# Performance work log

Measured on AMD Instinct MI355X. Metric: run time of the kernel, lower is better.

## Reference

```python
import jax, jax.numpy as jnp
import numpy as np

N_ENT = 100000
N_USR = 1024
E = 400000
D = 128
H = 4
R = 32


def setup_inputs() -> dict:
    key = jax.random.key(0)
    ks = jax.random.split(key, 9)
    a = float(np.sqrt(6.0 / (D + D)))  # xavier_uniform bound for [D, D]
    return {
        "entity_emb": jax.random.normal(ks[0], (N_ENT, D), dtype=jnp.float32),
        "user_emb": jax.random.normal(ks[1], (N_USR, D), dtype=jnp.float32),
        "interact_mat": jnp.zeros((1,), dtype=jnp.float32),  # unused by forward
        "weight": jax.random.normal(ks[2], (R, D), dtype=jnp.float32) * 0.1,
        "qTrans": jax.random.uniform(ks[3], (D, D), minval=-a, maxval=a, dtype=jnp.float32),
        "kTrans": jax.random.uniform(ks[4], (D, D), minval=-a, maxval=a, dtype=jnp.float32),
        "vTrans": jax.random.uniform(ks[5], (D, D), minval=-a, maxval=a, dtype=jnp.float32),
        "edge_index": jax.random.randint(ks[6], (2, E), 0, N_ENT, dtype=jnp.int64)
            if jax.config.jax_enable_x64 else jax.random.randint(ks[6], (2, E), 0, N_ENT, dtype=jnp.int32),
        "edge_type": jax.random.randint(ks[7], (E,), 1, R + 1, dtype=jnp.int32),  # types in [1, R]
        "layer": 0,
    }


def _kglayer(rows, col_embeds, embeds, n_seg, qT, kT, vT):
    # rows: [E] target-node index, col_embeds: [E, D] edge messages
    dh = D // H
    row_embeds = embeds[rows]                              # gather [E, D]
    q = (row_embeds @ qT).reshape(-1, H, dh)
    k = (col_embeds @ kT).reshape(-1, H, dh)
    v = (col_embeds @ vT).reshape(-1, H, dh)
    att = jnp.clip(jnp.einsum("ehd,ehd->eh", q, k), -10.0, 10.0)
    exp_att = jnp.exp(att)                                 # [E, H]
    att_norm = jax.ops.segment_sum(exp_att, rows, num_segments=n_seg)[rows]
    att = exp_att / (att_norm + 1e-8)
    res = (att[..., None] * v).reshape(-1, D)              # [E, D]
    return jax.ops.segment_sum(res, rows, num_segments=n_seg)


def _sim_hrt(head_emb, tail_emb, rel_emb):
    # per-edge scalar attention logit [E, 1]
    tr = jnp.linalg.norm(tail_emb * rel_emb, axis=1, keepdims=True)
    hr = jnp.linalg.norm(head_emb * rel_emb, axis=1, keepdims=True)
    return (hr * tr) ** 2


def reference(entity_emb, user_emb, interact_mat, weight, qTrans, kTrans, vTrans,
              edge_index, edge_type, layer):
    n_entities = entity_emb.shape[0]
    head, tail = edge_index[0], edge_index[1]
    rel = weight[edge_type - 1]                            # [E, D]
    neigh = entity_emb[tail] * rel                         # [E, D]
    kg_emb = _kglayer(head, neigh, entity_emb, n_entities, qTrans, kTrans, vTrans)
    w = _sim_hrt(kg_emb[head], kg_emb[tail], rel)          # [E, 1]
    w = jnp.broadcast_to(w, neigh.shape)                   # expand to [E, D]
    # scatter_softmax over edges sharing the same head (numerically stable)
    m = jax.ops.segment_max(w, head, num_segments=n_entities)[head]
    e = jnp.exp(w - m)
    s = jax.ops.segment_sum(e, head, num_segments=n_entities)[head]
    soft = e / s
    msg = soft * entity_emb[tail]
    return jax.ops.segment_sum(msg, head, num_segments=n_entities)
```

## Files before the change

kernel.cpp:

```cpp
#include <hip/hip_runtime.h>
#include <cstdint>

#define D 128
#define H 4
#define N_ENT 100000
#define N_EDGE 400000
#define R 32

#define SCAN_NB ((N_ENT + 511) / 512)

__global__ void k_hist(const int* __restrict__ head, int* __restrict__ deg) {
  const int e = blockIdx.x * 256 + threadIdx.x;
  if (e < N_EDGE) atomicAdd(&deg[head[e]], 1);
}

__global__ __launch_bounds__(256) void k_scan1(const int* __restrict__ deg,
                                               int* __restrict__ bsum) {
  const int t = threadIdx.x;
  const int i = blockIdx.x * 512 + t * 2;
  int v0 = (i < N_ENT) ? deg[i] : 0;
  int v1 = (i + 1 < N_ENT) ? deg[i + 1] : 0;
  int s = v0 + v1;
#pragma unroll
  for (int k = 1; k < 64; k <<= 1) s += __shfl_xor(s, k);
  __shared__ int ws[4];
  if ((t & 63) == 0) ws[t >> 6] = s;
  __syncthreads();
  if (t == 0) bsum[blockIdx.x] = ws[0] + ws[1] + ws[2] + ws[3];
}

__global__ __launch_bounds__(256) void k_scan2(const int* __restrict__ bsum,
                                               int* __restrict__ bbase,
                                               int* __restrict__ off) {
  __shared__ int sh[256];
  const int t = threadIdx.x;
  const int v = (t < SCAN_NB) ? bsum[t] : 0;
  sh[t] = v;
  __syncthreads();
  for (int d = 1; d < 256; d <<= 1) {
    const int u = (t >= d) ? sh[t - d] : 0;
    __syncthreads();
    sh[t] += u;
    __syncthreads();
  }
  if (t < SCAN_NB) bbase[t] = sh[t] - v;
  if (t == SCAN_NB - 1) off[N_ENT] = sh[t];
}

__global__ __launch_bounds__(256) void k_scan3(const int* __restrict__ deg,
                                               const int* __restrict__ bbase,
                                               int* __restrict__ off,
                                               int* __restrict__ cur) {
  __shared__ int sh[256];
  const int t = threadIdx.x;
  const int i = blockIdx.x * 512 + t * 2;
  const int v0 = (i < N_ENT) ? deg[i] : 0;
  const int v1 = (i + 1 < N_ENT) ? deg[i + 1] : 0;
  const int s = v0 + v1;
  sh[t] = s;
  __syncthreads();
  for (int d = 1; d < 256; d <<= 1) {
    const int u = (t >= d) ? sh[t - d] : 0;
    __syncthreads();
    sh[t] += u;
    __syncthreads();
  }
  const int ex = sh[t] - s + bbase[blockIdx.x];
  if (i < N_ENT) {
    off[i] = ex;
    cur[i] = ex;
  }
  if (i + 1 < N_ENT) {
    off[i + 1] = ex + v0;
    cur[i + 1] = ex + v0;
  }
}

__global__ void k_scatter(const int* __restrict__ head,
                          const int* __restrict__ tail,
                          const int* __restrict__ etype, int* __restrict__ cur,
                          int2* __restrict__ teP) {
  const int e = blockIdx.x * 256 + threadIdx.x;
  if (e >= N_EDGE) return;
  const int hd = head[e];
  const int pos = atomicAdd(&cur[hd], 1);
  teP[pos] = make_int2(tail[e], etype[e] - 1);
}

__global__ __launch_bounds__(256) void k_tr(const float* __restrict__ in,
                                            float* __restrict__ out) {
  __shared__ float tile[32][33];
  const int bx = blockIdx.x & 3, by = blockIdx.x >> 2;
  const int c = threadIdx.x & 31;
  const int r0 = (threadIdx.x >> 5) * 4;
#pragma unroll
  for (int i = 0; i < 4; ++i)
    tile[r0 + i][c] = in[(by * 32 + r0 + i) * 128 + bx * 32 + c];
  __syncthreads();
#pragma unroll
  for (int i = 0; i < 4; ++i)
    out[(bx * 32 + r0 + i) * 128 + by * 32 + c] = tile[c][r0 + i];
}

__global__ __launch_bounds__(512) void k_qproj(const float* __restrict__ ent,
                                               const float* __restrict__ qT,
                                               float* __restrict__ Q) {
  __shared__ float sT[D * D];
  __shared__ float rows[D * 128];
  const int t = threadIdx.x;
  const int n0 = blockIdx.x * 128;
#pragma unroll
  for (int s = 0; s < 8; ++s) {
    const int idx = (s * 512 + t) * 4;
    *(float4*)&sT[idx] = *(const float4*)&qT[idx];
  }
  {
    const int g = t & 3;
    const int n = t >> 2;
    const int node = n0 + n;
    if (node < N_ENT) {
      const float* src = ent + (size_t)node * D;
#pragma unroll
      for (int s = 0; s < 8; ++s) {
        const int i = s * 16 + g * 4;
        float4 v = *(const float4*)&src[i];
        rows[(i + 0) * 128 + n] = v.x;
        rows[(i + 1) * 128 + n] = v.y;
        rows[(i + 2) * 128 + n] = v.z;
        rows[(i + 3) * 128 + n] = v.w;
      }
    } else {
#pragma unroll
      for (int s = 0; s < 8; ++s) {
        const int i = s * 16 + g * 4;
        rows[(i + 0) * 128 + n] = 0.f;
        rows[(i + 1) * 128 + n] = 0.f;
        rows[(i + 2) * 128 + n] = 0.f;
        rows[(i + 3) * 128 + n] = 0.f;
      }
    }
  }
  __syncthreads();
  const int jj = t & 15;
  const int ee = t >> 4;
  float acc[4][8];
#pragma unroll
  for (int a = 0; a < 4; ++a)
#pragma unroll
    for (int b = 0; b < 8; ++b) acc[a][b] = 0.f;
#pragma unroll 4
  for (int i = 0; i < D; ++i) {
    float4 b0 = *(float4*)&sT[i * D + jj * 8];
    float4 b1 = *(float4*)&sT[i * D + jj * 8 + 4];
    float4 a0 = *(float4*)&rows[i * 128 + ee * 4];
    float bv[8] = {b0.x, b0.y, b0.z, b0.w, b1.x, b1.y, b1.z, b1.w};
    float av[4] = {a0.x, a0.y, a0.z, a0.w};
#pragma unroll
    for (int a = 0; a < 4; ++a)
#pragma unroll
      for (int b = 0; b < 8; ++b) acc[a][b] = fmaf(av[a], bv[b], acc[a][b]);
  }
#pragma unroll
  for (int a = 0; a < 4; ++a) {
    const int node = n0 + ee * 4 + a;
    if (node < N_ENT) {
      float4 o0 = {acc[a][0], acc[a][1], acc[a][2], acc[a][3]};
      float4 o1 = {acc[a][4], acc[a][5], acc[a][6], acc[a][7]};
      *(float4*)&Q[(size_t)node * D + jj * 8] = o0;
      *(float4*)&Q[(size_t)node * D + jj * 8 + 4] = o1;
    }
  }
}

__global__ __launch_bounds__(256, 8) void k_fused(
    const float* __restrict__ ent, const float* __restrict__ wrel,
    const float* __restrict__ kTt, const float* __restrict__ vT, float* qkg,
    const int* __restrict__ off, const int2* __restrict__ teP) {
  __shared__ float sQ[8 * 128];
  __shared__ float sPA[8 * 512];
  const int t = threadIdx.x;
  const int base = blockIdx.x * 8;

  const int wid = t >> 6;
  const int half = (t >> 5) & 1;
  const int l32 = t & 31;
  const int kk = wid * 2 + half;
  const int n = base + kk;

  {
    const int k = t >> 5;
    const int c4 = (t & 31) * 4;
    *(float4*)&sQ[k * 128 + c4] =
        *(const float4*)&qkg[(size_t)(base + k) * D + c4];
  }

  const int eb = off[n];
  const int deg = off[n + 1] - eb;
  float4 xv = {0, 0, 0, 0}, rv = {0, 0, 0, 0};
  if (deg > 0) {
    const int2 pf = teP[eb];
    xv = *(const float4*)&ent[(size_t)pf.x * D + l32 * 4];
    rv = *(const float4*)&wrel[(size_t)pf.y * D + l32 * 4];
  }
  __syncthreads();

  {
    const int i = t & 127;
    const int sub = t >> 7;
    float pp[2][8];
#pragma unroll
    for (int hh = 0; hh < 2; ++hh)
#pragma unroll
      for (int k = 0; k < 8; ++k) pp[hh][k] = 0.f;
#pragma unroll
    for (int hh = 0; hh < 2; ++hh) {
      const int h = sub * 2 + hh;
#pragma unroll 2
      for (int c4 = 0; c4 < 8; ++c4) {
        const float kv0 = kTt[(h * 32 + c4 * 4 + 0) * 128 + i];
        const float kv1 = kTt[(h * 32 + c4 * 4 + 1) * 128 + i];
        const float kv2 = kTt[(h * 32 + c4 * 4 + 2) * 128 + i];
        const float kv3 = kTt[(h * 32 + c4 * 4 + 3) * 128 + i];
#pragma unroll
        for (int k = 0; k < 8; ++k) {
          const float4 q = *(const float4*)&sQ[k * 128 + h * 32 + c4 * 4];
          pp[hh][k] = fmaf(kv0, q.x, pp[hh][k]);
          pp[hh][k] = fmaf(kv1, q.y, pp[hh][k]);
          pp[hh][k] = fmaf(kv2, q.z, pp[hh][k]);
          pp[hh][k] = fmaf(kv3, q.w, pp[hh][k]);
        }
      }
    }
#pragma unroll
    for (int hh = 0; hh < 2; ++hh)
#pragma unroll
      for (int k = 0; k < 8; ++k)
        sPA[k * 512 + (sub * 2 + hh) * 128 + i] = pp[hh][k];
  }
  __syncthreads();

  {
    const int lp = l32 & 3;
    const float4 P0 = *(const float4*)&sPA[kk * 512 + 0 * 128 + l32 * 4];
    const float4 P1 = *(const float4*)&sPA[kk * 512 + 1 * 128 + l32 * 4];
    const float4 P2 = *(const float4*)&sPA[kk * 512 + 2 * 128 + l32 * 4];
    const float4 P3 = *(const float4*)&sPA[kk * 512 + 3 * 128 + l32 * 4];
    float4 b0 = {0, 0, 0, 0}, b1 = {0, 0, 0, 0};
    float4 b2 = {0, 0, 0, 0}, b3 = {0, 0, 0, 0};
    float s0 = 0.f, s1 = 0.f, s2 = 0.f, s3 = 0.f;
    for (int idx = 0; idx < deg; ++idx) {
      const float4 cx = xv, cr = rv;
      if (idx + 1 < deg) {
        const int2 pf = teP[eb + idx + 1];
        xv = *(const float4*)&ent[(size_t)pf.x * D + l32 * 4];
        rv = *(const float4*)&wrel[(size_t)pf.y * D + l32 * 4];
      }
      const float4 nh = {cx.x * cr.x, cx.y * cr.y, cx.z * cr.z, cx.w * cr.w};
      float d0 = nh.x * P0.x + nh.y * P0.y + nh.z * P0.z + nh.w * P0.w;
      float d1 = nh.x * P1.x + nh.y * P1.y + nh.z * P1.z + nh.w * P1.w;
      float d2 = nh.x * P2.x + nh.y * P2.y + nh.z * P2.z + nh.w * P2.w;
      float d3 = nh.x * P3.x + nh.y * P3.y + nh.z * P3.z + nh.w * P3.w;
      float x01 = (l32 & 1) ? d1 : d0;
      float y01 = (l32 & 1) ? d0 : d1;
      x01 += __shfl_xor(y01, 1);
      float x23 = (l32 & 1) ? d3 : d2;
      float y23 = (l32 & 1) ? d2 : d3;
      x23 += __shfl_xor(y23, 1);
      float xa = (l32 & 2) ? x23 : x01;
      float xb = (l32 & 2) ? x01 : x23;
      xa += __shfl_xor(xb, 2);
      xa += __shfl_xor(xa, 4);
      xa += __shfl_xor(xa, 8);
      xa += __shfl_xor(xa, 16);
      const float eL = __expf(fminf(fmaxf(xa, -10.f), 10.f));
      const float e0 = eL;
      const float e1 = __shfl_xor(eL, 1);
      const float e2 = __shfl_xor(eL, 2);
      const float e3 = __shfl_xor(eL, 3);
      b0.x = fmaf(e0, nh.x, b0.x); b0.y = fmaf(e0, nh.y, b0.y);
      b0.z = fmaf(e0, nh.z, b0.z); b0.w = fmaf(e0, nh.w, b0.w);
      b1.x = fmaf(e1, nh.x, b1.x); b1.y = fmaf(e1, nh.y, b1.y);
      b1.z = fmaf(e1, nh.z, b1.z); b1.w = fmaf(e1, nh.w, b1.w);
      b2.x = fmaf(e2, nh.x, b2.x); b2.y = fmaf(e2, nh.y, b2.y);
      b2.z = fmaf(e2, nh.z, b2.z); b2.w = fmaf(e2, nh.w, b2.w);
      b3.x = fmaf(e3, nh.x, b3.x); b3.y = fmaf(e3, nh.y, b3.y);
      b3.z = fmaf(e3, nh.z, b3.z); b3.w = fmaf(e3, nh.w, b3.w);
      s0 += e0; s1 += e1; s2 += e2; s3 += e3;
    }
    const float i0 = 1.f / (s0 + 1e-8f);
    const float i1 = 1.f / (s1 + 1e-8f);
    const float i2 = 1.f / (s2 + 1e-8f);
    const float i3 = 1.f / (s3 + 1e-8f);
    float4 o0 = {b0.x * i0, b0.y * i0, b0.z * i0, b0.w * i0};
    float4 o1 = {b1.x * i1, b1.y * i1, b1.z * i1, b1.w * i1};
    float4 o2 = {b2.x * i2, b2.y * i2, b2.z * i2, b2.w * i2};
    float4 o3 = {b3.x * i3, b3.y * i3, b3.z * i3, b3.w * i3};
    const int sb = kk * 512 + l32 * 4;
    *(float4*)&sPA[sb + ((lp ^ 0) << 7)] = o0;
    *(float4*)&sPA[sb + ((lp ^ 1) << 7)] = o1;
    *(float4*)&sPA[sb + ((lp ^ 2) << 7)] = o2;
    *(float4*)&sPA[sb + ((lp ^ 3) << 7)] = o3;
  }
  __syncthreads();

  {
    const int c = t & 127;
    const int g4 = (t >> 7) * 4;
    const int h = c >> 5;
    float acc0 = 0.f, acc1 = 0.f, acc2 = 0.f, acc3 = 0.f;
    const float* agg0 = &sPA[(g4 + 0) * 512 + h * 128];
    const float* agg1 = &sPA[(g4 + 1) * 512 + h * 128];
    const float* agg2 = &sPA[(g4 + 2) * 512 + h * 128];
    const float* agg3 = &sPA[(g4 + 3) * 512 + h * 128];
#pragma unroll 4
    for (int d4 = 0; d4 < 32; ++d4) {
      const float4 a0 = *(const float4*)&agg0[d4 * 4];
      const float4 a1 = *(const float4*)&agg1[d4 * 4];
      const float4 a2 = *(const float4*)&agg2[d4 * 4];
      const float4 a3 = *(const float4*)&agg3[d4 * 4];
      const float v0 = vT[(d4 * 4 + 0) * 128 + c];
      const float v1 = vT[(d4 * 4 + 1) * 128 + c];
      const float v2 = vT[(d4 * 4 + 2) * 128 + c];
      const float v3 = vT[(d4 * 4 + 3) * 128 + c];
      acc0 = fmaf(a0.x, v0, acc0); acc0 = fmaf(a0.y, v1, acc0);
      acc0 = fmaf(a0.z, v2, acc0); acc0 = fmaf(a0.w, v3, acc0);
      acc1 = fmaf(a1.x, v0, acc1); acc1 = fmaf(a1.y, v1, acc1);
      acc1 = fmaf(a1.z, v2, acc1); acc1 = fmaf(a1.w, v3, acc1);
      acc2 = fmaf(a2.x, v0, acc2); acc2 = fmaf(a2.y, v1, acc2);
      acc2 = fmaf(a2.z, v2, acc2); acc2 = fmaf(a2.w, v3, acc2);
      acc3 = fmaf(a3.x, v0, acc3); acc3 = fmaf(a3.y, v1, acc3);
      acc3 = fmaf(a3.z, v2, acc3); acc3 = fmaf(a3.w, v3, acc3);
    }
    qkg[(size_t)(base + g4 + 0) * D + c] = acc0;
    qkg[(size_t)(base + g4 + 1) * D + c] = acc1;
    qkg[(size_t)(base + g4 + 2) * D + c] = acc2;
    qkg[(size_t)(base + g4 + 3) * D + c] = acc3;
  }
}

__global__ __launch_bounds__(256) void k_S(const float* __restrict__ kg,
                                           const float* __restrict__ wrel,
                                           float* __restrict__ S) {
  __shared__ float sB[D * 32];
  __shared__ float sA[D * 64];
  const int t = threadIdx.x;
  const int n0 = blockIdx.x * 64;
  {
    const int r = t & 31;
    const int qg = t >> 5;
#pragma unroll
    for (int s = 0; s < 4; ++s) {
      const int d = qg * 16 + s * 4;
      float4 b = *(const float4*)&wrel[(size_t)r * D + d];
      sB[(d + 0) * 32 + r] = b.x * b.x;
      sB[(d + 1) * 32 + r] = b.y * b.y;
      sB[(d + 2) * 32 + r] = b.z * b.z;
      sB[(d + 3) * 32 + r] = b.w * b.w;
    }
  }
  {
    const int nn = t & 63;
    const int dg = t >> 6;
    const int node = n0 + nn;
#pragma unroll
    for (int s = 0; s < 8; ++s) {
      const int d = dg * 32 + s * 4;
      float4 a = {0, 0, 0, 0};
      if (node < N_ENT) a = *(const float4*)&kg[(size_t)node * D + d];
      sA[(d + 0) * 64 + nn] = a.x * a.x;
      sA[(d + 1) * 64 + nn] = a.y * a.y;
      sA[(d + 2) * 64 + nn] = a.z * a.z;
      sA[(d + 3) * 64 + nn] = a.w * a.w;
    }
  }
  __syncthreads();
  const int nn2 = t >> 2;
  const int rg = t & 3;
  float acc[8];
#pragma unroll
  for (int c = 0; c < 8; ++c) acc[c] = 0.f;
#pragma unroll 4
  for (int d = 0; d < D; ++d) {
    const float a = sA[d * 64 + nn2];
    float4 b0 = *(float4*)&sB[d * 32 + rg * 8];
    float4 b1 = *(float4*)&sB[d * 32 + rg * 8 + 4];
    acc[0] = fmaf(a, b0.x, acc[0]);
    acc[1] = fmaf(a, b0.y, acc[1]);
    acc[2] = fmaf(a, b0.z, acc[2]);
    acc[3] = fmaf(a, b0.w, acc[3]);
    acc[4] = fmaf(a, b1.x, acc[4]);
    acc[5] = fmaf(a, b1.y, acc[5]);
    acc[6] = fmaf(a, b1.z, acc[6]);
    acc[7] = fmaf(a, b1.w, acc[7]);
  }
  const int node = n0 + nn2;
  if (node < N_ENT) {
    float4 o0 = {acc[0], acc[1], acc[2], acc[3]};
    float4 o1 = {acc[4], acc[5], acc[6], acc[7]};
    *(float4*)&S[(size_t)node * 32 + rg * 8] = o0;
    *(float4*)&S[(size_t)node * 32 + rg * 8 + 4] = o1;
  }
}

__global__ __launch_bounds__(256) void k_out2(
    const float* __restrict__ ent, const float* __restrict__ S,
    const int* __restrict__ off, const int2* __restrict__ teP,
    float* __restrict__ out) {
  const int t = threadIdx.x;
  const int wid = t >> 6;
  const int lane = t & 63;
  const int n = blockIdx.x * 4 + wid;
  if (n >= N_ENT) return;
  const int eb = off[n];
  const int deg = off[n + 1] - eb;
  float accx = 0.f, accy = 0.f;
  float m = 0.f, ssum = 0.f;
  for (int b = 0; b < deg; b += 64) {
    const int idx = b + lane;
    const bool val = idx < deg;
    const int e = eb + (val ? idx : 0);
    const int2 tp = teP[e];
    const int tl = tp.x;
    const int ty = tp.y;
    float w = val ? S[(size_t)n * 32 + ty] * S[(size_t)tl * 32 + ty] : -1.f;
    float cm = w;
#pragma unroll
    for (int k = 1; k < 64; k <<= 1) cm = fmaxf(cm, __shfl_xor(cm, k));
    const float mnew = fmaxf(m, cm);
    const float scale = __expf(m - mnew);
    const float el = val ? __expf(w - mnew) : 0.f;
    float cs = el;
#pragma unroll
    for (int k = 1; k < 64; k <<= 1) cs += __shfl_xor(cs, k);
    ssum = ssum * scale + cs;
    accx *= scale;
    accy *= scale;
    const int cnt = (deg - b < 64) ? deg - b : 64;
    {
      const int tl0 = __shfl(tl, 0);
      float2 xr = *(const float2*)&ent[(size_t)tl0 * D + lane * 2];
      for (int j = 0; j < cnt; ++j) {
        const float sj = __shfl(el, j);
        const float2 cx = xr;
        if (j + 1 < cnt) {
          const int tlj = __shfl(tl, j + 1);
          xr = *(const float2*)&ent[(size_t)tlj * D + lane * 2];
        }
        accx = fmaf(sj, cx.x, accx);
        accy = fmaf(sj, cx.y, accy);
      }
    }
    m = mnew;
  }
  const float inv = (deg > 0) ? 1.f / ssum : 0.f;
  float2 o = {accx * inv, accy * inv};
  *(float2*)&out[(size_t)n * D + lane * 2] = o;
}

extern "C" void kernel_launch(void* const* d_in, const int* in_sizes, int n_in,
                              void* d_out, int out_size, void* d_ws,
                              size_t ws_size, hipStream_t stream) {
  const float* ent = (const float*)d_in[0];
  const float* wrel = (const float*)d_in[3];
  const float* qT = (const float*)d_in[4];
  const float* kT = (const float*)d_in[5];
  const float* vT = (const float*)d_in[6];
  const int* eidx = (const int*)d_in[7];
  const int* etype = (const int*)d_in[8];
  const int* head = eidx;
  const int* tail = eidx + N_EDGE;

  float* S = (float*)d_ws;
  int* off = (int*)(S + (size_t)N_ENT * 32);
  int* cur = off + (N_ENT + 2);
  int* deg = cur + N_ENT;
  int* bsum = deg + N_ENT;
  int* bbase = bsum + SCAN_NB;
  int2* teP = (int2*)(bbase + SCAN_NB);
  float* kTt = (float*)(teP + N_EDGE);
  float* qkg = (float*)d_out;

  hipMemsetAsync(deg, 0, N_ENT * sizeof(int), stream);
  k_hist<<<(N_EDGE + 255) / 256, 256, 0, stream>>>(head, deg);
  k_scan1<<<SCAN_NB, 256, 0, stream>>>(deg, bsum);
  k_scan2<<<1, 256, 0, stream>>>(bsum, bbase, off);
  k_scan3<<<SCAN_NB, 256, 0, stream>>>(deg, bbase, off, cur);
  k_scatter<<<(N_EDGE + 255) / 256, 256, 0, stream>>>(head, tail, etype, cur,
                                                      teP);
  k_tr<<<16, 256, 0, stream>>>(kT, kTt);
  k_qproj<<<(N_ENT + 127) / 128, 512, 0, stream>>>(ent, qT, qkg);
  k_fused<<<N_ENT / 8, 256, 0, stream>>>(ent, wrel, kTt, vT, qkg, off, teP);
  k_S<<<(N_ENT + 63) / 64, 256, 0, stream>>>(qkg, wrel, S);
  k_out2<<<(N_ENT + 3) / 4, 256, 0, stream>>>(ent, S, off, teP, qkg);
}
```

Baseline: 512.1 us.

## Fuse relation-similarity matrix into attention kernel and narrow output gather to half-waves

The per-node S = kg^2 · wrel^2 computation moves into the tail of k_fused, using squared kg values kept in shared memory, so the kg embedding no longer round-trips through global memory for a separate k_S launch. Squared relation weights are precomputed once in a merged prep kernel that reuses the transpose launch. k_out2 now handles 8 nodes per block with 32-lane groups using float4 loads instead of 64-lane float2. The P vectors are also reloaded from LDS each iteration rather than held in registers, which may lower register pressure but adds LDS traffic. The S dot product in k_fused is unblocked (one scalar per thread over 128 values), which costs extra ALU and LDS work in that kernel.

```diff
diff --git a/kernel.cpp b/kernel.cpp
--- a/kernel.cpp
+++ b/kernel.cpp
@@ -87,19 +87,32 @@
   teP[pos] = make_int2(tail[e], etype[e] - 1);
 }
 
-__global__ __launch_bounds__(256) void k_tr(const float* __restrict__ in,
-                                            float* __restrict__ out) {
-  __shared__ float tile[32][33];
-  const int bx = blockIdx.x & 3, by = blockIdx.x >> 2;
-  const int c = threadIdx.x & 31;
-  const int r0 = (threadIdx.x >> 5) * 4;
-#pragma unroll
-  for (int i = 0; i < 4; ++i)
-    tile[r0 + i][c] = in[(by * 32 + r0 + i) * 128 + bx * 32 + c];
-  __syncthreads();
-#pragma unroll
-  for (int i = 0; i < 4; ++i)
-    out[(bx * 32 + r0 + i) * 128 + by * 32 + c] = tile[c][r0 + i];
+__global__ __launch_bounds__(256) void k_prep(const float* __restrict__ kT,
+                                              float* __restrict__ kTt,
+                                              const float* __restrict__ wrel,
+                                              float* __restrict__ wrel2) {
+  if (blockIdx.x < 16) {
+    __shared__ float tile[32][33];
+    const int bx = blockIdx.x & 3, by = blockIdx.x >> 2;
+    const int c = threadIdx.x & 31;
+    const int r0 = (threadIdx.x >> 5) * 4;
+#pragma unroll
+    for (int i = 0; i < 4; ++i)
+      tile[r0 + i][c] = kT[(by * 32 + r0 + i) * 128 + bx * 32 + c];
+    __syncthreads();
+#pragma unroll
+    for (int i = 0; i < 4; ++i)
+      kTt[(bx * 32 + r0 + i) * 128 + by * 32 + c] = tile[c][r0 + i];
+  } else {
+    const int t = threadIdx.x;
+#pragma unroll
+    for (int s = 0; s < 4; ++s) {
+      const int idx = (s * 256 + t) * 4;
+      float4 v = *(const float4*)&wrel[idx];
+      v.x *= v.x; v.y *= v.y; v.z *= v.z; v.w *= v.w;
+      *(float4*)&wrel2[idx] = v;
+    }
+  }
 }
 
 __global__ __launch_bounds__(512) void k_qproj(const float* __restrict__ ent,
@@ -174,13 +187,14 @@
 
 __global__ __launch_bounds__(256, 8) void k_fused(
     const float* __restrict__ ent, const float* __restrict__ wrel,
-    const float* __restrict__ kTt, const float* __restrict__ vT, float* qkg,
-    const int* __restrict__ off, const int2* __restrict__ teP) {
+    const float* __restrict__ kTt, const float* __restrict__ vT,
+    const float* __restrict__ wrel2, const float* __restrict__ qkg,
+    float* __restrict__ S, const int* __restrict__ off,
+    const int2* __restrict__ teP) {
   __shared__ float sQ[8 * 128];
   __shared__ float sPA[8 * 512];
   const int t = threadIdx.x;
   const int base = blockIdx.x * 8;
-
   const int wid = t >> 6;
   const int half = (t >> 5) & 1;
   const int l32 = t & 31;
@@ -241,25 +255,25 @@
 
   {
     const int lp = l32 & 3;
-    const float4 P0 = *(const float4*)&sPA[kk * 512 + 0 * 128 + l32 * 4];
-    const float4 P1 = *(const float4*)&sPA[kk * 512 + 1 * 128 + l32 * 4];
-    const float4 P2 = *(const float4*)&sPA[kk * 512 + 2 * 128 + l32 * 4];
-    const float4 P3 = *(const float4*)&sPA[kk * 512 + 3 * 128 + l32 * 4];
+    const float* Pb = &sPA[kk * 512 + l32 * 4];
     float4 b0 = {0, 0, 0, 0}, b1 = {0, 0, 0, 0};
     float4 b2 = {0, 0, 0, 0}, b3 = {0, 0, 0, 0};
     float s0 = 0.f, s1 = 0.f, s2 = 0.f, s3 = 0.f;
     for (int idx = 0; idx < deg; ++idx) {
-      const float4 cx = xv, cr = rv;
+      const float4 nh = {xv.x * rv.x, xv.y * rv.y, xv.z * rv.z, xv.w * rv.w};
       if (idx + 1 < deg) {
         const int2 pf = teP[eb + idx + 1];
         xv = *(const float4*)&ent[(size_t)pf.x * D + l32 * 4];
         rv = *(const float4*)&wrel[(size_t)pf.y * D + l32 * 4];
       }
-      const float4 nh = {cx.x * cr.x, cx.y * cr.y, cx.z * cr.z, cx.w * cr.w};
-      float d0 = nh.x * P0.x + nh.y * P0.y + nh.z * P0.z + nh.w * P0.w;
-      float d1 = nh.x * P1.x + nh.y * P1.y + nh.z * P1.z + nh.w * P1.w;
-      float d2 = nh.x * P2.x + nh.y * P2.y + nh.z * P2.z + nh.w * P2.w;
-      float d3 = nh.x * P3.x + nh.y * P3.y + nh.z * P3.z + nh.w * P3.w;
+      const float4 p0 = *(const float4*)&Pb[0];
+      const float4 p1 = *(const float4*)&Pb[128];
+      const float4 p2 = *(const float4*)&Pb[256];
+      const float4 p3 = *(const float4*)&Pb[384];
+      float d0 = nh.x * p0.x + nh.y * p0.y + nh.z * p0.z + nh.w * p0.w;
+      float d1 = nh.x * p1.x + nh.y * p1.y + nh.z * p1.z + nh.w * p1.w;
+      float d2 = nh.x * p2.x + nh.y * p2.y + nh.z * p2.z + nh.w * p2.w;
+      float d3 = nh.x * p3.x + nh.y * p3.y + nh.z * p3.z + nh.w * p3.w;
       float x01 = (l32 & 1) ? d1 : d0;
       float y01 = (l32 & 1) ? d0 : d1;
       x01 += __shfl_xor(y01, 1);
@@ -331,74 +345,27 @@
       acc3 = fmaf(a3.x, v0, acc3); acc3 = fmaf(a3.y, v1, acc3);
       acc3 = fmaf(a3.z, v2, acc3); acc3 = fmaf(a3.w, v3, acc3);
     }
-    qkg[(size_t)(base + g4 + 0) * D + c] = acc0;
-    qkg[(size_t)(base + g4 + 1) * D + c] = acc1;
-    qkg[(size_t)(base + g4 + 2) * D + c] = acc2;
-    qkg[(size_t)(base + g4 + 3) * D + c] = acc3;
-  }
-}
-
-__global__ __launch_bounds__(256) void k_S(const float* __restrict__ kg,
-                                           const float* __restrict__ wrel,
-                                           float* __restrict__ S) {
-  __shared__ float sB[D * 32];
-  __shared__ float sA[D * 64];
-  const int t = threadIdx.x;
-  const int n0 = blockIdx.x * 64;
-  {
+    sQ[(g4 + 0) * 128 + c] = acc0 * acc0;
+    sQ[(g4 + 1) * 128 + c] = acc1 * acc1;
+    sQ[(g4 + 2) * 128 + c] = acc2 * acc2;
+    sQ[(g4 + 3) * 128 + c] = acc3 * acc3;
+  }
+  __syncthreads();
+
+  {
+    const int nn = t >> 5;
     const int r = t & 31;
-    const int qg = t >> 5;
-#pragma unroll
-    for (int s = 0; s < 4; ++s) {
-      const int d = qg * 16 + s * 4;
-      float4 b = *(const float4*)&wrel[(size_t)r * D + d];
-      sB[(d + 0) * 32 + r] = b.x * b.x;
-      sB[(d + 1) * 32 + r] = b.y * b.y;
-      sB[(d + 2) * 32 + r] = b.z * b.z;
-      sB[(d + 3) * 32 + r] = b.w * b.w;
-    }
-  }
-  {
-    const int nn = t & 63;
-    const int dg = t >> 6;
-    const int node = n0 + nn;
-#pragma unroll
-    for (int s = 0; s < 8; ++s) {
-      const int d = dg * 32 + s * 4;
-      float4 a = {0, 0, 0, 0};
-      if (node < N_ENT) a = *(const float4*)&kg[(size_t)node * D + d];
-      sA[(d + 0) * 64 + nn] = a.x * a.x;
-      sA[(d + 1) * 64 + nn] = a.y * a.y;
-      sA[(d + 2) * 64 + nn] = a.z * a.z;
-      sA[(d + 3) * 64 + nn] = a.w * a.w;
-    }
-  }
-  __syncthreads();
-  const int nn2 = t >> 2;
-  const int rg = t & 3;
-  float acc[8];
-#pragma unroll
-  for (int c = 0; c < 8; ++c) acc[c] = 0.f;
+    const float* kg2 = &sQ[nn * 128];
+    const float* w2 = &wrel2[r * 128];
+    float acc = 0.f;
 #pragma unroll 4
-  for (int d = 0; d < D; ++d) {
-    const float a = sA[d * 64 + nn2];
-    float4 b0 = *(float4*)&sB[d * 32 + rg * 8];
-    float4 b1 = *(float4*)&sB[d * 32 + rg * 8 + 4];
-    acc[0] = fmaf(a, b0.x, acc[0]);
-    acc[1] = fmaf(a, b0.y, acc[1]);
-    acc[2] = fmaf(a, b0.z, acc[2]);
-    acc[3] = fmaf(a, b0.w, acc[3]);
-    acc[4] = fmaf(a, b1.x, acc[4]);
-    acc[5] = fmaf(a, b1.y, acc[5]);
-    acc[6] = fmaf(a, b1.z, acc[6]);
-    acc[7] = fmaf(a, b1.w, acc[7]);
-  }
-  const int node = n0 + nn2;
-  if (node < N_ENT) {
-    float4 o0 = {acc[0], acc[1], acc[2], acc[3]};
-    float4 o1 = {acc[4], acc[5], acc[6], acc[7]};
-    *(float4*)&S[(size_t)node * 32 + rg * 8] = o0;
-    *(float4*)&S[(size_t)node * 32 + rg * 8 + 4] = o1;
+    for (int c4 = 0; c4 < 32; ++c4) {
+      const float4 a = *(const float4*)&kg2[c4 * 4];
+      const float4 b = *(const float4*)&w2[c4 * 4];
+      acc = fmaf(a.x, b.x, acc); acc = fmaf(a.y, b.y, acc);
+      acc = fmaf(a.z, b.z, acc); acc = fmaf(a.w, b.w, acc);
+    }
+    S[(size_t)(base + nn) * 32 + r] = acc;
   }
 }
 
@@ -408,15 +375,17 @@
     float* __restrict__ out) {
   const int t = threadIdx.x;
   const int wid = t >> 6;
-  const int lane = t & 63;
-  const int n = blockIdx.x * 4 + wid;
+  const int half = (t >> 5) & 1;
+  const int l32 = t & 31;
+  const int kk = wid * 2 + half;
+  const int n = blockIdx.x * 8 + kk;
   if (n >= N_ENT) return;
   const int eb = off[n];
   const int deg = off[n + 1] - eb;
-  float accx = 0.f, accy = 0.f;
+  float4 acc = {0, 0, 0, 0};
   float m = 0.f, ssum = 0.f;
-  for (int b = 0; b < deg; b += 64) {
-    const int idx = b + lane;
+  for (int b = 0; b < deg; b += 32) {
+    const int idx = b + l32;
     const bool val = idx < deg;
     const int e = eb + (val ? idx : 0);
     const int2 tp = teP[e];
@@ -425,36 +394,37 @@
     float w = val ? S[(size_t)n * 32 + ty] * S[(size_t)tl * 32 + ty] : -1.f;
     float cm = w;
 #pragma unroll
-    for (int k = 1; k < 64; k <<= 1) cm = fmaxf(cm, __shfl_xor(cm, k));
+    for (int k = 1; k < 32; k <<= 1) cm = fmaxf(cm, __shfl_xor(cm, k));
     const float mnew = fmaxf(m, cm);
     const float scale = __expf(m - mnew);
     const float el = val ? __expf(w - mnew) : 0.f;
     float cs = el;
 #pragma unroll
-    for (int k = 1; k < 64; k <<= 1) cs += __shfl_xor(cs, k);
+    for (int k = 1; k < 32; k <<= 1) cs += __shfl_xor(cs, k);
     ssum = ssum * scale + cs;
-    accx *= scale;
-    accy *= scale;
-    const int cnt = (deg - b < 64) ? deg - b : 64;
+    acc.x *= scale; acc.y *= scale; acc.z *= scale; acc.w *= scale;
+    const int cnt = (deg - b < 32) ? deg - b : 32;
     {
-      const int tl0 = __shfl(tl, 0);
-      float2 xr = *(const float2*)&ent[(size_t)tl0 * D + lane * 2];
+      const int tl0 = __shfl(tl, 0, 32);
+      float4 xr = *(const float4*)&ent[(size_t)tl0 * D + l32 * 4];
       for (int j = 0; j < cnt; ++j) {
-        const float sj = __shfl(el, j);
-        const float2 cx = xr;
+        const float sj = __shfl(el, j, 32);
+        const float4 cx = xr;
         if (j + 1 < cnt) {
-          const int tlj = __shfl(tl, j + 1);
-          xr = *(const float2*)&ent[(size_t)tlj * D + lane * 2];
+          const int tlj = __shfl(tl, j + 1, 32);
+          xr = *(const float4*)&ent[(size_t)tlj * D + l32 * 4];
         }
-        accx = fmaf(sj, cx.x, accx);
-        accy = fmaf(sj, cx.y, accy);
+        acc.x = fmaf(sj, cx.x, acc.x);
+        acc.y = fmaf(sj, cx.y, acc.y);
+        acc.z = fmaf(sj, cx.z, acc.z);
+        acc.w = fmaf(sj, cx.w, acc.w);
       }
     }
     m = mnew;
   }
   const float inv = (deg > 0) ? 1.f / ssum : 0.f;
-  float2 o = {accx * inv, accy * inv};
-  *(float2*)&out[(size_t)n * D + lane * 2] = o;
+  float4 o = {acc.x * inv, acc.y * inv, acc.z * inv, acc.w * inv};
+  *(float4*)&out[(size_t)n * D + l32 * 4] = o;
 }
 
 extern "C" void kernel_launch(void* const* d_in, const int* in_sizes, int n_in,
@@ -478,6 +448,7 @@
   int* bbase = bsum + SCAN_NB;
   int2* teP = (int2*)(bbase + SCAN_NB);
   float* kTt = (float*)(teP + N_EDGE);
+  float* wrel2 = (float*)cur;
   float* qkg = (float*)d_out;
 
   hipMemsetAsync(deg, 0, N_ENT * sizeof(int), stream);
@@ -487,9 +458,9 @@
   k_scan3<<<SCAN_NB, 256, 0, stream>>>(deg, bbase, off, cur);
   k_scatter<<<(N_EDGE + 255) / 256, 256, 0, stream>>>(head, tail, etype, cur,
                                                       teP);
-  k_tr<<<16, 256, 0, stream>>>(kT, kTt);
+  k_prep<<<17, 256, 0, stream>>>(kT, kTt, wrel, wrel2);
   k_qproj<<<(N_ENT + 127) / 128, 512, 0, stream>>>(ent, qT, qkg);
-  k_fused<<<N_ENT / 8, 256, 0, stream>>>(ent, wrel, kTt, vT, qkg, off, teP);
-  k_S<<<(N_ENT + 63) / 64, 256, 0, stream>>>(qkg, wrel, S);
-  k_out2<<<(N_ENT + 3) / 4, 256, 0, stream>>>(ent, S, off, teP, qkg);
-}
+  k_fused<<<N_ENT / 8, 256, 0, stream>>>(ent, wrel, kTt, vT, wrel2, qkg, S,
+                                         off, teP);
+  k_out2<<<(N_ENT + 7) / 8, 256, 0, stream>>>(ent, S, off, teP, qkg);
+}
```

Result: slower. 638.0 us (+24.6%).

## Process two nodes per wavefront in output kernel with float4 gathers and 4-way unroll

Applied to the files above, without the earlier changes.

The final aggregation kernel now gives each node a 32-lane half-wave instead of a full 64-lane wave, so each wavefront handles two nodes. Each lane loads float4 instead of float2, and up to four neighbor rows are loaded before their FMAs are issued, raising memory-level parallelism. The head node's S row is loaded once into registers and read with a shuffle instead of a per-edge global load. Average degree is about 4, so this cuts idle lanes and serialized gathers, at the cost of more branches and width-32 shuffle reductions.

```diff
diff --git a/kernel.cpp b/kernel.cpp
--- a/kernel.cpp
+++ b/kernel.cpp
@@ -408,53 +408,78 @@
     float* __restrict__ out) {
   const int t = threadIdx.x;
   const int wid = t >> 6;
-  const int lane = t & 63;
-  const int n = blockIdx.x * 4 + wid;
+  const int half = (t >> 5) & 1;
+  const int l32 = t & 31;
+  const int kk = wid * 2 + half;
+  const int n = blockIdx.x * 8 + kk;
   if (n >= N_ENT) return;
   const int eb = off[n];
   const int deg = off[n + 1] - eb;
-  float accx = 0.f, accy = 0.f;
+  const float sn = S[(size_t)n * 32 + l32];
+  float4 acc = {0, 0, 0, 0};
   float m = 0.f, ssum = 0.f;
-  for (int b = 0; b < deg; b += 64) {
-    const int idx = b + lane;
+  for (int b = 0; b < deg; b += 32) {
+    const int idx = b + l32;
     const bool val = idx < deg;
     const int e = eb + (val ? idx : 0);
     const int2 tp = teP[e];
     const int tl = tp.x;
     const int ty = tp.y;
-    float w = val ? S[(size_t)n * 32 + ty] * S[(size_t)tl * 32 + ty] : -1.f;
+    const float snv = __shfl(sn, ty, 32);
+    float w = val ? snv * S[(size_t)tl * 32 + ty] : -1.f;
     float cm = w;
 #pragma unroll
-    for (int k = 1; k < 64; k <<= 1) cm = fmaxf(cm, __shfl_xor(cm, k));
+    for (int k = 1; k < 32; k <<= 1) cm = fmaxf(cm, __shfl_xor(cm, k));
     const float mnew = fmaxf(m, cm);
     const float scale = __expf(m - mnew);
     const float el = val ? __expf(w - mnew) : 0.f;
     float cs = el;
 #pragma unroll
-    for (int k = 1; k < 64; k <<= 1) cs += __shfl_xor(cs, k);
+    for (int k = 1; k < 32; k <<= 1) cs += __shfl_xor(cs, k);
     ssum = ssum * scale + cs;
-    accx *= scale;
-    accy *= scale;
-    const int cnt = (deg - b < 64) ? deg - b : 64;
-    {
-      const int tl0 = __shfl(tl, 0);
-      float2 xr = *(const float2*)&ent[(size_t)tl0 * D + lane * 2];
-      for (int j = 0; j < cnt; ++j) {
-        const float sj = __shfl(el, j);
-        const float2 cx = xr;
-        if (j + 1 < cnt) {
-          const int tlj = __shfl(tl, j + 1);
-          xr = *(const float2*)&ent[(size_t)tlj * D + lane * 2];
-        }
-        accx = fmaf(sj, cx.x, accx);
-        accy = fmaf(sj, cx.y, accy);
+    acc.x *= scale; acc.y *= scale; acc.z *= scale; acc.w *= scale;
+    const int cnt = (deg - b < 32) ? deg - b : 32;
+    for (int j0 = 0; j0 < cnt; j0 += 4) {
+      const int rem = cnt - j0;
+      const int t0 = __shfl(tl, j0 + 0, 32);
+      float4 r0 = *(const float4*)&ent[(size_t)t0 * D + l32 * 4];
+      float4 r1, r2, r3;
+      if (rem > 1) {
+        const int t1 = __shfl(tl, j0 + 1, 32);
+        r1 = *(const float4*)&ent[(size_t)t1 * D + l32 * 4];
+      }
+      if (rem > 2) {
+        const int t2 = __shfl(tl, j0 + 2, 32);
+        r2 = *(const float4*)&ent[(size_t)t2 * D + l32 * 4];
+      }
+      if (rem > 3) {
+        const int t3 = __shfl(tl, j0 + 3, 32);
+        r3 = *(const float4*)&ent[(size_t)t3 * D + l32 * 4];
+      }
+      const float w0 = __shfl(el, j0 + 0, 32);
+      acc.x = fmaf(w0, r0.x, acc.x); acc.y = fmaf(w0, r0.y, acc.y);
+      acc.z = fmaf(w0, r0.z, acc.z); acc.w = fmaf(w0, r0.w, acc.w);
+      if (rem > 1) {
+        const float w1 = __shfl(el, j0 + 1, 32);
+        acc.x = fmaf(w1, r1.x, acc.x); acc.y = fmaf(w1, r1.y, acc.y);
+        acc.z = fmaf(w1, r1.z, acc.z); acc.w = fmaf(w1, r1.w, acc.w);
+      }
+      if (rem > 2) {
+        const float w2 = __shfl(el, j0 + 2, 32);
+        acc.x = fmaf(w2, r2.x, acc.x); acc.y = fmaf(w2, r2.y, acc.y);
+        acc.z = fmaf(w2, r2.z, acc.z); acc.w = fmaf(w2, r2.w, acc.w);
+      }
+      if (rem > 3) {
+        const float w3 = __shfl(el, j0 + 3, 32);
+        acc.x = fmaf(w3, r3.x, acc.x); acc.y = fmaf(w3, r3.y, acc.y);
+        acc.z = fmaf(w3, r3.z, acc.z); acc.w = fmaf(w3, r3.w, acc.w);
       }
     }
     m = mnew;
   }
   const float inv = (deg > 0) ? 1.f / ssum : 0.f;
-  float2 o = {accx * inv, accy * inv};
-  *(float2*)&out[(size_t)n * D + lane * 2] = o;
+  float4 o = {acc.x * inv, acc.y * inv, acc.z * inv, acc.w * inv};
+  *(float4*)&out[(size_t)n * D + l32 * 4] = o;
 }
 
 extern "C" void kernel_launch(void* const* d_in, const int* in_sizes, int n_in,
@@ -491,5 +516,5 @@
   k_qproj<<<(N_ENT + 127) / 128, 512, 0, stream>>>(ent, qT, qkg);
   k_fused<<<N_ENT / 8, 256, 0, stream>>>(ent, wrel, kTt, vT, qkg, off, teP);
   k_S<<<(N_ENT + 63) / 64, 256, 0, stream>>>(qkg, wrel, S);
-  k_out2<<<(N_ENT + 3) / 4, 256, 0, stream>>>(ent, S, off, teP, qkg);
-}
+  k_out2<<<(N_ENT + 7) / 8, 256, 0, stream>>>(ent, S, off, teP, qkg);
+}
```

Measured after the change: 504.1 us, median of 2. About the same (-1.6%).
